# Optimization experiments

Measured on AMD Instinct MI355X. Metric: run time of the kernel, lower is better.

The kernel has to match this reference:

```python
import jax, jax.numpy as jnp
import numpy as np

N_NODES = 100000


def gcn_conv(x, src, dst, W, b):
    # PyG GCNConv: add self-loops, symmetric deg^-1/2 normalization,
    # linear transform, scatter-add aggregation to target nodes, plus bias.
    n = x.shape[0]
    loops = jnp.arange(n, dtype=src.dtype)
    s = jnp.concatenate([src, loops])
    d = jnp.concatenate([dst, loops])
    deg = jax.ops.segment_sum(jnp.ones_like(s, dtype=x.dtype), d, num_segments=n)
    dinv = jnp.where(deg > 0, jax.lax.rsqrt(deg), 0.0)
    norm = dinv[s] * dinv[d]                       # [E+n]
    h = x @ W                                      # [n, out]
    msg = h[s] * norm[:, None]                     # gather + scale
    out = jax.ops.segment_sum(msg, d, num_segments=n)
    return out + b


def setup_inputs() -> dict:
    key = jax.random.key(0)
    k1, k2, k3, k4 = jax.random.split(key, 4)
    in_c, hid_c, out_c = 64, 64, 64
    n_edges = 1600000
    x = jax.random.normal(k1, (N_NODES, in_c), dtype=jnp.float32)
    edge_index = jax.random.randint(k2, (2, n_edges), 0, N_NODES, dtype=jnp.int64)
    W1 = jax.random.normal(k3, (in_c, hid_c), dtype=jnp.float32) * (1.0 / np.sqrt(in_c))
    b1 = jnp.zeros((hid_c,), dtype=jnp.float32)
    W2 = jax.random.normal(k4, (hid_c, out_c), dtype=jnp.float32) * (1.0 / np.sqrt(hid_c))
    b2 = jnp.zeros((out_c,), dtype=jnp.float32)
    return {"x": x, "edge_index": edge_index, "W1": W1, "b1": b1, "W2": W2, "b2": b2}


def reference(x, edge_index, W1, b1, W2, b2):
    src, dst = edge_index[0], edge_index[1]
    h = gcn_conv(x, src, dst, W1, b1)
    h = jax.nn.relu(h)
    out = gcn_conv(h, src, dst, W2, b2)
    return out
```

## Files before the change

kernel.cpp:

```cpp
#include <hip/hip_runtime.h>

#define NCH 64
#define NBLK 512
#define CB 512

typedef unsigned int uint;
typedef short short8 __attribute__((ext_vector_type(8)));
typedef float floatx4 __attribute__((ext_vector_type(4)));

__device__ inline uint bf16rne(float f) {
    uint u = __float_as_uint(f);
    return (u + 0x7fffu + ((u >> 16) & 1u)) >> 16;
}
__device__ inline uint pack2bf(float lo, float hi) {
    return bf16rne(lo) | (bf16rne(hi) << 16);
}
__device__ inline float unpLo(uint v) { return __uint_as_float(v << 16); }
__device__ inline float unpHi(uint v) { return __uint_as_float(v & 0xffff0000u); }


__global__ void coarse_hist_kernel(const int* __restrict__ dst, int* __restrict__ cntCB,
                                   int ne, int epb) {
    __shared__ int h[CB];
    int t = threadIdx.x;
    for (int i = t; i < CB; i += blockDim.x) h[i] = 0;
    __syncthreads();
    int e0 = blockIdx.x * epb;
    int e1 = min(e0 + epb, ne);
    for (int e = e0 + t; e < e1; e += blockDim.x)
        atomicAdd(&h[dst[e] >> 8], 1);
    __syncthreads();
    for (int i = t; i < CB; i += blockDim.x) cntCB[i * NBLK + blockIdx.x] = h[i];
}

__global__ void binscan_kernel(int* __restrict__ cntCB, int* __restrict__ binTot) {
    __shared__ int s[NBLK];
    int bin = blockIdx.x;
    int t = threadIdx.x;
    int v = cntCB[bin * NBLK + t];
    s[t] = v;
    __syncthreads();
    for (int off = 1; off < NBLK; off <<= 1) {
        int add = (t >= off) ? s[t - off] : 0;
        __syncthreads();
        s[t] += add;
        __syncthreads();
    }
    cntCB[bin * NBLK + t] = s[t] - v;
    if (t == NBLK - 1) binTot[bin] = s[t];
}

__global__ void cbscan_kernel(const int* __restrict__ binTot, int* __restrict__ cb,
                              int* __restrict__ rowptr, int n, int ne) {
    __shared__ int s[CB];
    int t = threadIdx.x;
    int v = binTot[t];
    s[t] = v;
    __syncthreads();
    for (int off = 1; off < CB; off <<= 1) {
        int add = (t >= off) ? s[t - off] : 0;
        __syncthreads();
        s[t] += add;
        __syncthreads();
    }
    cb[t] = s[t] - v;
    if (t == CB - 1) { cb[CB] = ne; rowptr[n] = ne; }
}

__global__ void coarse_scatter_kernel(const int* __restrict__ src, const int* __restrict__ dst,
                                      const int* __restrict__ cntCB, const int* __restrict__ cb,
                                      int2* __restrict__ coarse, int ne, int epb) {
    __shared__ int cur[CB];
    int t = threadIdx.x;
    for (int i = t; i < CB; i += blockDim.x)
        cur[i] = cb[i] + cntCB[i * NBLK + blockIdx.x];
    __syncthreads();
    int e0 = blockIdx.x * epb;
    int e1 = min(e0 + epb, ne);
    for (int e = e0 + t; e < e1; e += blockDim.x) {
        int d = dst[e];
        int pos = atomicAdd(&cur[d >> 8], 1);
        coarse[pos] = make_int2(d, src[e]);
    }
}

__global__ void bucket_kernel(const int2* __restrict__ coarse, const int* __restrict__ cb,
                              int* __restrict__ rowptr, float* __restrict__ dinv,
                              int* __restrict__ csr, int n) {
    __shared__ int hist[256];
    __shared__ int excl[256];
    __shared__ int cursor[256];
    int k = blockIdx.x;
    int t = threadIdx.x;
    int base = cb[k];
    int end = cb[k + 1];
    hist[t] = 0;
    __syncthreads();
    for (int i = base + t; i < end; i += 256)
        atomicAdd(&hist[coarse[i].x & 255], 1);
    __syncthreads();
    int v = hist[t];
    excl[t] = v;
    __syncthreads();
    for (int off = 1; off < 256; off <<= 1) {
        int add = (t >= off) ? excl[t - off] : 0;
        __syncthreads();
        excl[t] += add;
        __syncthreads();
    }
    int ex = excl[t] - v;
    int node = (k << 8) + t;
    if (node < n) {
        rowptr[node] = base + ex;
        dinv[node] = rsqrtf(1.0f + (float)v);
    }
    cursor[t] = base + ex;
    __syncthreads();
    for (int i = base + t; i < end; i += 256) {
        int2 e = coarse[i];
        int pos = atomicAdd(&cursor[e.x & 255], 1);
        csr[pos] = e.y;
    }
}

__global__ void wfrag_kernel(const float* __restrict__ W1, const float* __restrict__ W2,
                             uint4* __restrict__ frag) {
    int tid = blockIdx.x * blockDim.x + threadIdx.x;
    if (tid >= 1024) return;
    int mat = tid >> 9;
    int rem = tid & 511;
    int nt = rem >> 7;
    int kb = (rem >> 6) & 1;
    int lane = rem & 63;
    const float* W = mat ? W2 : W1;
    int kbase = kb * 32 + (lane >> 4) * 8;
    int col = nt * 16 + (lane & 15);
    uint r[4];
#pragma unroll
    for (int j = 0; j < 4; ++j) {
        float lo = W[(kbase + 2 * j) * NCH + col];
        float hi = W[(kbase + 2 * j + 1) * NCH + col];
        r[j] = pack2bf(lo, hi);
    }
    frag[tid] = make_uint4(r[0], r[1], r[2], r[3]);
}

template<bool BF16A>
__global__ void gemm_mfma_kernel(const void* __restrict__ Xv, const uint4* __restrict__ wfrag,
                                 const float* __restrict__ dinv, uint* __restrict__ H, int n) {
    int lane = threadIdx.x & 63;
    int wave = blockIdx.x * (blockDim.x >> 6) + (threadIdx.x >> 6);
    int rb = wave * 16;
    if (rb >= n) return;

    short8 bfrag[4][2];
#pragma unroll
    for (int nt = 0; nt < 4; ++nt)
#pragma unroll
        for (int kb = 0; kb < 2; ++kb) {
            uint4 u = wfrag[(nt * 2 + kb) * 64 + lane];
            bfrag[nt][kb] = *(short8*)&u;
        }

    short8 afrag[2];
    if (BF16A) {
        const uint* hr = (const uint*)Xv + (long long)(rb + (lane & 15)) * 32 + (lane >> 4) * 8;
        uint4 a0 = *(const uint4*)(hr);
        uint4 a1 = *(const uint4*)(hr + 4);
        uint w[8] = {a0.x, a0.y, a0.z, a0.w, a1.x, a1.y, a1.z, a1.w};
        short8 f0, f1;
#pragma unroll
        for (int j = 0; j < 8; ++j) {
            f0[j] = (short)(w[j] & 0xffffu);
            f1[j] = (short)(w[j] >> 16);
        }
        afrag[0] = f0;
        afrag[1] = f1;
    } else {
        const float* xr = (const float*)Xv + (long long)(rb + (lane & 15)) * NCH + (lane >> 4) * 8;
#pragma unroll
        for (int kb = 0; kb < 2; ++kb) {
            float4 v0 = *(const float4*)(xr + kb * 32);
            float4 v1 = *(const float4*)(xr + kb * 32 + 4);
            short8 a;
            a[0] = (short)bf16rne(v0.x); a[1] = (short)bf16rne(v0.y);
            a[2] = (short)bf16rne(v0.z); a[3] = (short)bf16rne(v0.w);
            a[4] = (short)bf16rne(v1.x); a[5] = (short)bf16rne(v1.y);
            a[6] = (short)bf16rne(v1.z); a[7] = (short)bf16rne(v1.w);
            afrag[kb] = a;
        }
    }

    floatx4 acc[4];
#pragma unroll
    for (int nt = 0; nt < 4; ++nt) acc[nt] = (floatx4){0.f, 0.f, 0.f, 0.f};
#pragma unroll
    for (int nt = 0; nt < 4; ++nt)
#pragma unroll
        for (int kb = 0; kb < 2; ++kb)
            acc[nt] = __builtin_amdgcn_mfma_f32_16x16x32_bf16(afrag[kb], bfrag[nt][kb], acc[nt], 0, 0, 0);

    int r0 = rb + (lane >> 4) * 4;
#pragma unroll
    for (int reg = 0; reg < 4; ++reg) {
        float di = dinv[r0 + reg];
        long long roww = (long long)(r0 + reg) * 32;
#pragma unroll
        for (int nt = 0; nt < 2; ++nt) {
            int w = nt * 16 + (lane & 15);
            H[roww + w] = pack2bf(di * acc[nt][reg], di * acc[nt + 2][reg]);
        }
    }
}

template<bool BF16OUT>
__global__ void agg_kernel(const uint* __restrict__ hsB, const int* __restrict__ rowptr,
                           const int* __restrict__ csr, const float* __restrict__ dinv,
                           const float* __restrict__ b, void* __restrict__ outv, int n) {
    int wid = (blockIdx.x * blockDim.x + threadIdx.x) >> 6;
    if (wid >= n) return;
    wid = __builtin_amdgcn_readfirstlane(wid);
    int lane = threadIdx.x & 63;
    int q = lane >> 4;
    int u = lane & 15;
    int start = rowptr[wid];
    int end = rowptr[wid + 1];
    const uint2* __restrict__ base = (const uint2*)hsB + u;
    float ax0 = 0.f, ax1 = 0.f, ay0 = 0.f, ay1 = 0.f;
    if (q == 0) {
        uint2 v = base[(long long)wid * 16];
        ax0 = unpLo(v.x); ay0 = unpHi(v.x); ax1 = unpLo(v.y); ay1 = unpHi(v.y);
    }
    int eb = start;
    for (; eb + 32 <= end; eb += 32) {
        int4 i0, i1;
        __builtin_memcpy(&i0, csr + eb + 4 * q, 16);
        __builtin_memcpy(&i1, csr + eb + 16 + 4 * q, 16);
        uint2 v0 = base[(long long)i0.x * 16];
        uint2 v1 = base[(long long)i0.y * 16];
        uint2 v2 = base[(long long)i0.z * 16];
        uint2 v3 = base[(long long)i0.w * 16];
        uint2 v4 = base[(long long)i1.x * 16];
        uint2 v5 = base[(long long)i1.y * 16];
        uint2 v6 = base[(long long)i1.z * 16];
        uint2 v7 = base[(long long)i1.w * 16];
        ax0 += ((unpLo(v0.x) + unpLo(v1.x)) + (unpLo(v2.x) + unpLo(v3.x)))
             + ((unpLo(v4.x) + unpLo(v5.x)) + (unpLo(v6.x) + unpLo(v7.x)));
        ay0 += ((unpHi(v0.x) + unpHi(v1.x)) + (unpHi(v2.x) + unpHi(v3.x)))
             + ((unpHi(v4.x) + unpHi(v5.x)) + (unpHi(v6.x) + unpHi(v7.x)));
        ax1 += ((unpLo(v0.y) + unpLo(v1.y)) + (unpLo(v2.y) + unpLo(v3.y)))
             + ((unpLo(v4.y) + unpLo(v5.y)) + (unpLo(v6.y) + unpLo(v7.y)));
        ay1 += ((unpHi(v0.y) + unpHi(v1.y)) + (unpHi(v2.y) + unpHi(v3.y)))
             + ((unpHi(v4.y) + unpHi(v5.y)) + (unpHi(v6.y) + unpHi(v7.y)));
    }
    if (eb < end) {
        int4 i0, i1;
        __builtin_memcpy(&i0, csr + eb + 4 * q, 16);
        __builtin_memcpy(&i1, csr + eb + 16 + 4 * q, 16);
        int s[8] = {i0.x, i0.y, i0.z, i0.w, i1.x, i1.y, i1.z, i1.w};
#pragma unroll
        for (int k = 0; k < 8; ++k) {
            int idx = eb + 16 * (k >> 2) + 4 * q + (k & 3);
            bool c = idx < end;
            int sk = c ? s[k] : 0;
            uint2 v = base[(long long)sk * 16];
            ax0 += c ? unpLo(v.x) : 0.f;
            ay0 += c ? unpHi(v.x) : 0.f;
            ax1 += c ? unpLo(v.y) : 0.f;
            ay1 += c ? unpHi(v.y) : 0.f;
        }
    }
    ax0 += __shfl_xor(ax0, 16, 64); ay0 += __shfl_xor(ay0, 16, 64);
    ax1 += __shfl_xor(ax1, 16, 64); ay1 += __shfl_xor(ay1, 16, 64);
    ax0 += __shfl_xor(ax0, 32, 64); ay0 += __shfl_xor(ay0, 32, 64);
    ax1 += __shfl_xor(ax1, 32, 64); ay1 += __shfl_xor(ay1, 32, 64);
    if (q == 0) {
        float d = dinv[wid];
        float2 blo = *(const float2*)(b + 2 * u);
        float2 bhi = *(const float2*)(b + 2 * u + 32);
        float r00 = d * ax0 + blo.x;
        float r01 = d * ax1 + blo.y;
        float r10 = d * ay0 + bhi.x;
        float r11 = d * ay1 + bhi.y;
        if (BF16OUT) {
            uint w0 = pack2bf(fmaxf(r00, 0.f), fmaxf(r10, 0.f));
            uint w1 = pack2bf(fmaxf(r01, 0.f), fmaxf(r11, 0.f));
            *((uint2*)outv + (long long)wid * 16 + u) = make_uint2(w0, w1);
        } else {
            float* out = (float*)outv;
            *(float2*)(out + (long long)wid * NCH + 2 * u) = make_float2(r00, r01);
            *(float2*)(out + (long long)wid * NCH + 2 * u + 32) = make_float2(r10, r11);
        }
    }
}

extern "C" void kernel_launch(void* const* d_in, const int* in_sizes, int n_in,
                              void* d_out, int out_size, void* d_ws, size_t ws_size,
                              hipStream_t stream) {
    const float* x  = (const float*)d_in[0];
    const int*   ei = (const int*)d_in[1];
    const float* W1 = (const float*)d_in[2];
    const float* b1 = (const float*)d_in[3];
    const float* W2 = (const float*)d_in[4];
    const float* b2 = (const float*)d_in[5];
    const int n  = in_sizes[0] / NCH;
    const int ne = in_sizes[1] / 2;
    const int* src = ei;
    const int* dst = ei + ne;

    char* ws = (char*)d_ws;
    size_t off = 0;
    auto alloc = [&](size_t bytes) { void* p = ws + off; off += (bytes + 255) & ~(size_t)255; return p; };
    int*   cntCB   = (int*)alloc((size_t)CB * NBLK * 4);
    int*   binTot  = (int*)alloc((size_t)CB * 4);
    int*   cb      = (int*)alloc((size_t)(CB + 1) * 4);
    int*   rowptr  = (int*)alloc((size_t)(n + 1) * 4);
    float* dinv    = (float*)alloc((size_t)n * 4);
    int*   csr     = (int*)alloc((size_t)ne * 4 + 128);
    int2*  coarse  = (int2*)alloc((size_t)ne * 8);
    uint*  hsB     = (uint*)alloc((size_t)n * 32 * 4);
    uint*  hsB2    = (uint*)alloc((size_t)n * 32 * 4);
    uint4* wfrag   = (uint4*)alloc(1024 * 16);

    const int blk = 256;
    const int gAgg = (n * 64 + blk - 1) / blk;
    const int epb  = (ne + NBLK - 1) / NBLK;
    const int nBuck = (n + 255) / 256;
    const int nWaveG = (n + 15) / 16;
    const int gGemm = (nWaveG + 3) / 4;

    wfrag_kernel         <<<4, 256, 0, stream>>>(W1, W2, wfrag);
    coarse_hist_kernel   <<<NBLK, blk, 0, stream>>>(dst, cntCB, ne, epb);
    binscan_kernel       <<<CB, NBLK, 0, stream>>>(cntCB, binTot);
    cbscan_kernel        <<<1, CB, 0, stream>>>(binTot, cb, rowptr, n, ne);
    coarse_scatter_kernel<<<NBLK, blk, 0, stream>>>(src, dst, cntCB, cb, coarse, ne, epb);
    bucket_kernel        <<<nBuck, 256, 0, stream>>>(coarse, cb, rowptr, dinv, csr, n);

    gemm_mfma_kernel<false><<<gGemm, blk, 0, stream>>>(x, wfrag, dinv, hsB, n);
    agg_kernel<true><<<gAgg, blk, 0, stream>>>(hsB, rowptr, csr, dinv, b1, hsB2, n);

    gemm_mfma_kernel<true><<<gGemm, blk, 0, stream>>>(hsB2, wfrag + 512, dinv, hsB, n);
    agg_kernel<false><<<gAgg, blk, 0, stream>>>(hsB, rowptr, csr, dinv, b2, d_out, n);
}
```

Before: 158.2 us.

## Pack coarse edges into 32-bit words and widen aggregation gathers to 16B

The coarse bucket array now stores each edge as one 32-bit word, with the low 8 bits of dst in the top byte and src in the low 24 bits, halving its write and read traffic. The aggregation kernel now has each lane gather a full 16-byte row segment: eight lanes cover a row and eight edge groups are processed in parallel. Tails are handled by pointing out-of-range slots at a zeroed sentinel row n instead of using predicated adds. The extra wfrag block zeroes that sentinel row. Node ids must fit in 24 bits, and the reduction now needs three shuffle stages over eight accumulators.

```diff
diff --git a/kernel.cpp b/kernel.cpp
--- a/kernel.cpp
+++ b/kernel.cpp
@@ -69,7 +69,7 @@
 
 __global__ void coarse_scatter_kernel(const int* __restrict__ src, const int* __restrict__ dst,
                                       const int* __restrict__ cntCB, const int* __restrict__ cb,
-                                      int2* __restrict__ coarse, int ne, int epb) {
+                                      uint* __restrict__ coarse, int ne, int epb) {
     __shared__ int cur[CB];
     int t = threadIdx.x;
     for (int i = t; i < CB; i += blockDim.x)
@@ -80,11 +80,11 @@
     for (int e = e0 + t; e < e1; e += blockDim.x) {
         int d = dst[e];
         int pos = atomicAdd(&cur[d >> 8], 1);
-        coarse[pos] = make_int2(d, src[e]);
-    }
-}
-
-__global__ void bucket_kernel(const int2* __restrict__ coarse, const int* __restrict__ cb,
+        coarse[pos] = ((uint)(d & 255) << 24) | (uint)src[e];
+    }
+}
+
+__global__ void bucket_kernel(const uint* __restrict__ coarse, const int* __restrict__ cb,
                               int* __restrict__ rowptr, float* __restrict__ dinv,
                               int* __restrict__ csr, int n) {
     __shared__ int hist[256];
@@ -97,7 +97,7 @@
     hist[t] = 0;
     __syncthreads();
     for (int i = base + t; i < end; i += 256)
-        atomicAdd(&hist[coarse[i].x & 255], 1);
+        atomicAdd(&hist[coarse[i] >> 24], 1);
     __syncthreads();
     int v = hist[t];
     excl[t] = v;
@@ -117,16 +117,22 @@
     cursor[t] = base + ex;
     __syncthreads();
     for (int i = base + t; i < end; i += 256) {
-        int2 e = coarse[i];
-        int pos = atomicAdd(&cursor[e.x & 255], 1);
-        csr[pos] = e.y;
+        uint e = coarse[i];
+        int pos = atomicAdd(&cursor[e >> 24], 1);
+        csr[pos] = (int)(e & 0x00FFFFFFu);
     }
 }
 
 __global__ void wfrag_kernel(const float* __restrict__ W1, const float* __restrict__ W2,
-                             uint4* __restrict__ frag) {
+                             uint4* __restrict__ frag, uint* __restrict__ z1,
+                             uint* __restrict__ z2, int n) {
+    if (blockIdx.x == 4) {
+        int t = threadIdx.x;
+        if (t < 32) z1[(long long)n * 32 + t] = 0u;
+        else if (t < 64) z2[(long long)n * 32 + (t - 32)] = 0u;
+        return;
+    }
     int tid = blockIdx.x * blockDim.x + threadIdx.x;
-    if (tid >= 1024) return;
     int mat = tid >> 9;
     int rem = tid & 511;
     int nt = rem >> 7;
@@ -221,75 +227,65 @@
     if (wid >= n) return;
     wid = __builtin_amdgcn_readfirstlane(wid);
     int lane = threadIdx.x & 63;
-    int q = lane >> 4;
-    int u = lane & 15;
+    int o = lane >> 3;
+    int u = lane & 7;
     int start = rowptr[wid];
     int end = rowptr[wid + 1];
-    const uint2* __restrict__ base = (const uint2*)hsB + u;
-    float ax0 = 0.f, ax1 = 0.f, ay0 = 0.f, ay1 = 0.f;
-    if (q == 0) {
-        uint2 v = base[(long long)wid * 16];
-        ax0 = unpLo(v.x); ay0 = unpHi(v.x); ax1 = unpLo(v.y); ay1 = unpHi(v.y);
-    }
-    int eb = start;
-    for (; eb + 32 <= end; eb += 32) {
-        int4 i0, i1;
-        __builtin_memcpy(&i0, csr + eb + 4 * q, 16);
-        __builtin_memcpy(&i1, csr + eb + 16 + 4 * q, 16);
-        uint2 v0 = base[(long long)i0.x * 16];
-        uint2 v1 = base[(long long)i0.y * 16];
-        uint2 v2 = base[(long long)i0.z * 16];
-        uint2 v3 = base[(long long)i0.w * 16];
-        uint2 v4 = base[(long long)i1.x * 16];
-        uint2 v5 = base[(long long)i1.y * 16];
-        uint2 v6 = base[(long long)i1.z * 16];
-        uint2 v7 = base[(long long)i1.w * 16];
-        ax0 += ((unpLo(v0.x) + unpLo(v1.x)) + (unpLo(v2.x) + unpLo(v3.x)))
-             + ((unpLo(v4.x) + unpLo(v5.x)) + (unpLo(v6.x) + unpLo(v7.x)));
-        ay0 += ((unpHi(v0.x) + unpHi(v1.x)) + (unpHi(v2.x) + unpHi(v3.x)))
-             + ((unpHi(v4.x) + unpHi(v5.x)) + (unpHi(v6.x) + unpHi(v7.x)));
-        ax1 += ((unpLo(v0.y) + unpLo(v1.y)) + (unpLo(v2.y) + unpLo(v3.y)))
-             + ((unpLo(v4.y) + unpLo(v5.y)) + (unpLo(v6.y) + unpLo(v7.y)));
-        ay1 += ((unpHi(v0.y) + unpHi(v1.y)) + (unpHi(v2.y) + unpHi(v3.y)))
-             + ((unpHi(v4.y) + unpHi(v5.y)) + (unpHi(v6.y) + unpHi(v7.y)));
-    }
-    if (eb < end) {
-        int4 i0, i1;
-        __builtin_memcpy(&i0, csr + eb + 4 * q, 16);
-        __builtin_memcpy(&i1, csr + eb + 16 + 4 * q, 16);
-        int s[8] = {i0.x, i0.y, i0.z, i0.w, i1.x, i1.y, i1.z, i1.w};
-#pragma unroll
-        for (int k = 0; k < 8; ++k) {
-            int idx = eb + 16 * (k >> 2) + 4 * q + (k & 3);
-            bool c = idx < end;
-            int sk = c ? s[k] : 0;
-            uint2 v = base[(long long)sk * 16];
-            ax0 += c ? unpLo(v.x) : 0.f;
-            ay0 += c ? unpHi(v.x) : 0.f;
-            ax1 += c ? unpLo(v.y) : 0.f;
-            ay1 += c ? unpHi(v.y) : 0.f;
-        }
-    }
-    ax0 += __shfl_xor(ax0, 16, 64); ay0 += __shfl_xor(ay0, 16, 64);
-    ax1 += __shfl_xor(ax1, 16, 64); ay1 += __shfl_xor(ay1, 16, 64);
-    ax0 += __shfl_xor(ax0, 32, 64); ay0 += __shfl_xor(ay0, 32, 64);
-    ax1 += __shfl_xor(ax1, 32, 64); ay1 += __shfl_xor(ay1, 32, 64);
-    if (q == 0) {
+    const uint4* __restrict__ base = (const uint4*)hsB + u;
+    int ss = (o == 0) ? wid : n;
+    uint4 v = base[(long long)ss * 8];
+    float a0l = unpLo(v.x), a0h = unpHi(v.x);
+    float a1l = unpLo(v.y), a1h = unpHi(v.y);
+    float a2l = unpLo(v.z), a2h = unpHi(v.z);
+    float a3l = unpLo(v.w), a3h = unpHi(v.w);
+    for (int eb = start; eb < end; eb += 32) {
+        int s0 = csr[eb + o];
+        int s1 = csr[eb + 8 + o];
+        int s2 = csr[eb + 16 + o];
+        int s3 = csr[eb + 24 + o];
+        s0 = (eb + o      < end) ? s0 : n;
+        s1 = (eb + 8 + o  < end) ? s1 : n;
+        s2 = (eb + 16 + o < end) ? s2 : n;
+        s3 = (eb + 24 + o < end) ? s3 : n;
+        uint4 g0 = base[(long long)s0 * 8];
+        uint4 g1 = base[(long long)s1 * 8];
+        uint4 g2 = base[(long long)s2 * 8];
+        uint4 g3 = base[(long long)s3 * 8];
+        a0l += (unpLo(g0.x) + unpLo(g1.x)) + (unpLo(g2.x) + unpLo(g3.x));
+        a0h += (unpHi(g0.x) + unpHi(g1.x)) + (unpHi(g2.x) + unpHi(g3.x));
+        a1l += (unpLo(g0.y) + unpLo(g1.y)) + (unpLo(g2.y) + unpLo(g3.y));
+        a1h += (unpHi(g0.y) + unpHi(g1.y)) + (unpHi(g2.y) + unpHi(g3.y));
+        a2l += (unpLo(g0.z) + unpLo(g1.z)) + (unpLo(g2.z) + unpLo(g3.z));
+        a2h += (unpHi(g0.z) + unpHi(g1.z)) + (unpHi(g2.z) + unpHi(g3.z));
+        a3l += (unpLo(g0.w) + unpLo(g1.w)) + (unpLo(g2.w) + unpLo(g3.w));
+        a3h += (unpHi(g0.w) + unpHi(g1.w)) + (unpHi(g2.w) + unpHi(g3.w));
+    }
+#pragma unroll
+    for (int m = 8; m <= 32; m <<= 1) {
+        a0l += __shfl_xor(a0l, m, 64); a0h += __shfl_xor(a0h, m, 64);
+        a1l += __shfl_xor(a1l, m, 64); a1h += __shfl_xor(a1h, m, 64);
+        a2l += __shfl_xor(a2l, m, 64); a2h += __shfl_xor(a2h, m, 64);
+        a3l += __shfl_xor(a3l, m, 64); a3h += __shfl_xor(a3h, m, 64);
+    }
+    if (o == 0) {
         float d = dinv[wid];
-        float2 blo = *(const float2*)(b + 2 * u);
-        float2 bhi = *(const float2*)(b + 2 * u + 32);
-        float r00 = d * ax0 + blo.x;
-        float r01 = d * ax1 + blo.y;
-        float r10 = d * ay0 + bhi.x;
-        float r11 = d * ay1 + bhi.y;
+        float4 bl = *(const float4*)(b + 4 * u);
+        float4 bh = *(const float4*)(b + 4 * u + 32);
+        float r0l = d * a0l + bl.x, r1l = d * a1l + bl.y;
+        float r2l = d * a2l + bl.z, r3l = d * a3l + bl.w;
+        float r0h = d * a0h + bh.x, r1h = d * a1h + bh.y;
+        float r2h = d * a2h + bh.z, r3h = d * a3h + bh.w;
         if (BF16OUT) {
-            uint w0 = pack2bf(fmaxf(r00, 0.f), fmaxf(r10, 0.f));
-            uint w1 = pack2bf(fmaxf(r01, 0.f), fmaxf(r11, 0.f));
-            *((uint2*)outv + (long long)wid * 16 + u) = make_uint2(w0, w1);
+            uint4 w;
+            w.x = pack2bf(fmaxf(r0l, 0.f), fmaxf(r0h, 0.f));
+            w.y = pack2bf(fmaxf(r1l, 0.f), fmaxf(r1h, 0.f));
+            w.z = pack2bf(fmaxf(r2l, 0.f), fmaxf(r2h, 0.f));
+            w.w = pack2bf(fmaxf(r3l, 0.f), fmaxf(r3h, 0.f));
+            *((uint4*)outv + (long long)wid * 8 + u) = w;
         } else {
-            float* out = (float*)outv;
-            *(float2*)(out + (long long)wid * NCH + 2 * u) = make_float2(r00, r01);
-            *(float2*)(out + (long long)wid * NCH + 2 * u + 32) = make_float2(r10, r11);
+            float* out = (float*)outv + (long long)wid * NCH;
+            *(float4*)(out + 4 * u) = make_float4(r0l, r1l, r2l, r3l);
+            *(float4*)(out + 4 * u + 32) = make_float4(r0h, r1h, r2h, r3h);
         }
     }
 }
@@ -317,9 +313,9 @@
     int*   rowptr  = (int*)alloc((size_t)(n + 1) * 4);
     float* dinv    = (float*)alloc((size_t)n * 4);
     int*   csr     = (int*)alloc((size_t)ne * 4 + 128);
-    int2*  coarse  = (int2*)alloc((size_t)ne * 8);
-    uint*  hsB     = (uint*)alloc((size_t)n * 32 * 4);
-    uint*  hsB2    = (uint*)alloc((size_t)n * 32 * 4);
+    uint*  coarse  = (uint*)alloc((size_t)ne * 4);
+    uint*  hsB     = (uint*)alloc((size_t)(n + 1) * 32 * 4);
+    uint*  hsB2    = (uint*)alloc((size_t)(n + 1) * 32 * 4);
     uint4* wfrag   = (uint4*)alloc(1024 * 16);
 
     const int blk = 256;
@@ -329,7 +325,7 @@
     const int nWaveG = (n + 15) / 16;
     const int gGemm = (nWaveG + 3) / 4;
 
-    wfrag_kernel         <<<4, 256, 0, stream>>>(W1, W2, wfrag);
+    wfrag_kernel         <<<5, 256, 0, stream>>>(W1, W2, wfrag, hsB, hsB2, n);
     coarse_hist_kernel   <<<NBLK, blk, 0, stream>>>(dst, cntCB, ne, epb);
     binscan_kernel       <<<CB, NBLK, 0, stream>>>(cntCB, binTot);
     cbscan_kernel        <<<1, CB, 0, stream>>>(binTot, cb, rowptr, n, ne);
```

After: 145.5 us. 8.0% less time.
